# Optimization experiments

Hardware: AMD Instinct MI355X
Metric: run time of the kernel (lower is better)

Reference implementation:

```python
import jax, jax.numpy as jnp
import numpy as np

IN_DIM = 500
BATCH = 131072
NBSECTOR = 11
NBMQ = 10
X_THRESHOLD = 0.001
INF_SCALE = 100.0
ZSTAR = 1000.0
CARD_UPPER = 70.0
CARD_LOWER = 69.0


def setup_inputs() -> dict:
    key = jax.random.key(0)
    ks = jax.random.split(key, 7)
    x = jax.random.uniform(ks[0], (BATCH, IN_DIM), dtype=jnp.float32)
    x_bw = jax.random.uniform(ks[1], (IN_DIM,), dtype=jnp.float32)
    alpha = jax.random.normal(ks[2], (IN_DIM,), dtype=jnp.float32)
    beta = jax.random.normal(ks[3], (IN_DIM,), dtype=jnp.float32)
    # risk matrix: small-magnitude so the quadratic form dQd is in a sane range
    Omega = 0.001 * jax.random.normal(ks[4], (IN_DIM, IN_DIM), dtype=jnp.float32)
    sector_id = jax.random.randint(ks[5], (IN_DIM,), 0, NBSECTOR, dtype=jnp.int32)
    mq_id = jax.random.randint(ks[6], (IN_DIM,), 0, NBMQ, dtype=jnp.int32)
    return {"x": x, "x_bw": x_bw, "alpha": alpha, "beta": beta,
            "Omega": Omega, "sector_id": sector_id, "mq_id": mq_id}


def reference(x, x_bw, alpha, beta, Omega, sector_id, mq_id):
    relu = jax.nn.relu
    d = x - x_bw                      # [B, D]
    abs_d = jnp.abs(d)
    sx = jnp.sum(x, axis=1)           # [B]

    tot = relu(1.0 - sx) + relu(sx - 1.0)
    tot = tot + relu(jnp.sum(abs_d, axis=1) - 0.05)

    # per-group masked sums (replaces the one-hot matvec loops):
    # segment-sum over the feature axis, then |.|, relu, sum over groups.
    sec = jax.ops.segment_sum(d.T, sector_id, num_segments=NBSECTOR).T  # [B, NBSECTOR]
    tot = tot + jnp.sum(relu(jnp.abs(sec) - 0.1), axis=1)
    mqs = jax.ops.segment_sum(d.T, mq_id, num_segments=NBMQ).T          # [B, NBMQ]
    tot = tot + jnp.sum(relu(jnp.abs(mqs) - 0.1), axis=1)

    tot = tot + relu(jnp.abs(d @ beta) - 0.1)

    # eval-mode cardinality constraint (train=False branch): hard count
    nnz = jnp.sum((x > X_THRESHOLD).astype(x.dtype), axis=1)
    tot = tot + relu(nnz - CARD_UPPER) + relu(CARD_LOWER - nnz)

    # NOTE: original sums |d| over the WHOLE batch (scalar), faithfully kept
    l_all = 0.5 * jnp.sum(abs_d)
    tot = tot + relu(0.6 - l_all)

    dQd = jnp.sum((d @ Omega) * d, axis=1)  # quadratic form per row
    tot = tot + relu(dQd - 0.01) + relu(0.0025 - dQd)

    l2 = d @ alpha
    # MONTH == 0 branch of the original
    tot = tot + relu(100.0 * dQd - 100.0 * l2 - ZSTAR)

    fea_probs = relu(1.0 - jnp.tanh(tot / INF_SCALE))
    return fea_probs
```

## Files before the change

### kernel.cpp

```cpp
#include <hip/hip_runtime.h>
#include <hip/hip_bf16.h>

#define D_IN  500
#define BATCH 131072
#define BM    64

typedef unsigned short u16;
typedef unsigned int   u32;
using f32x4  = __attribute__((ext_vector_type(4))) float;
using bf16x8 = __attribute__((ext_vector_type(8))) short;

__device__ __forceinline__ u16 f2bf(float f) {
  u32 b = __builtin_bit_cast(u32, f);
  b += 0x7FFFu + ((b >> 16) & 1u);
  return (u16)(b >> 16);
}
__device__ __forceinline__ float bf2f(u32 hbits) {
  return __builtin_bit_cast(float, hbits << 16);
}

__device__ __forceinline__ float xla_tanh(float z) {
  float xc = fminf(fmaxf(z, -7.90531110764903f), 7.90531110764903f);
  float x2 = xc * xc;
  float p = fmaf(x2, -2.76076847742355e-16f, 2.00018790482477e-13f);
  p = fmaf(x2, p, -8.60467152213735e-11f);
  p = fmaf(x2, p,  5.12229709037114e-08f);
  p = fmaf(x2, p,  1.48572235717979e-05f);
  p = fmaf(x2, p,  6.37261928875436e-04f);
  p = fmaf(x2, p,  4.89352455891786e-03f);
  p = xc * p;
  float q = fmaf(x2, 1.19825839466702e-06f, 1.18534705686654e-04f);
  q = fmaf(x2, q, 2.26843463243900e-03f);
  q = fmaf(x2, q, 4.89352518554385e-03f);
  return (fabsf(z) < 0.0004f) ? z : (p / q);
}

__global__ void disc_prep(const float* __restrict__ Omega,
                          const float* __restrict__ alpha,
                          const float* __restrict__ beta,
                          const float* __restrict__ x_bw,
                          const int* __restrict__ sector_id,
                          const int* __restrict__ mq_id,
                          u16* __restrict__ wsA,
                          float* __restrict__ thr,
                          float* __restrict__ smalls) {
  int idx = blockIdx.x * 256 + threadIdx.x;
  if (idx == 1) smalls[1] = 0.0f;
  if (idx < 512) thr[idx] = (idx < D_IN) ? (0.001f - x_bw[idx]) : 3.0e38f;
  if (blockIdx.x == 0 && threadIdx.x < 64) {
    float s = 0.f;
    for (int c = threadIdx.x; c < D_IN; c += 64) s += x_bw[c];
    #pragma unroll
    for (int m = 1; m < 64; m <<= 1) s += __shfl_xor(s, m, 64);
    if (threadIdx.x == 0) smalls[0] = s;
  }
  if (idx >= 544 * 512) return;
  int blk    = idx >> 9;
  int within = idx & 511;
  int lane   = within >> 3;
  int e      = within & 7;
  int n, j;
  if (blk < 512) {
    int chunk = blk >> 5;
    int nw    = (blk >> 4) & 1;
    int jg    = (blk >> 2) & 3;
    int ks    = blk & 3;
    n = chunk * 32 + nw * 16 + (lane & 15);
    j = jg * 128 + ks * 32 + ((lane >> 4) << 3) + e;
  } else {
    int b4  = blk - 512;
    int sub = b4 >> 2;
    int ks  = b4 & 3;
    int nw = sub >> 2, jg = sub & 3;
    n = 512 + nw * 16 + (lane & 15);
    j = jg * 128 + ks * 32 + ((lane >> 4) << 3) + e;
  }
  float v = 0.0f;
  if (j < D_IN) {
    if (n < D_IN)       v = Omega[j * D_IN + n];
    else if (n < 512)   v = 0.0f;
    else if (n < 523)   v = (sector_id[j] == (n - 512)) ? 1.0f : 0.0f;
    else if (n < 533)   v = (mq_id[j]     == (n - 523)) ? 1.0f : 0.0f;
    else if (n == 533)  v = beta[j];
    else if (n == 534)  v = alpha[j];
    else if (n == 535)  v = 1.0f;
  }
  wsA[idx] = f2bf(v);
}

__global__ __launch_bounds__(512, 2) void disc_main(
    const float* __restrict__ x, const float* __restrict__ x_bw,
    const u16* __restrict__ wsA, const float* __restrict__ thr,
    const float* __restrict__ smalls,
    float* __restrict__ tot_out, float* __restrict__ l_all) {
  __shared__ alignas(16) u16 ldsA[BM * 512];
  __shared__ float s_ext[BM][25];
  __shared__ float s_dqd[BM][8];
  __shared__ float s_sabs[BM];
  __shared__ float s_nnz[BM];

  const int t = threadIdx.x;
  const float* xblk = x + (size_t)blockIdx.x * (BM * D_IN);

  for (int z = t; z < BM * 25; z += 512) ((float*)s_ext)[z] = 0.0f;
  if (t < BM) { s_sabs[t] = 0.0f; s_nnz[t] = 0.0f; }

  for (int z = t; z < BM * 12; z += 512) {
    int r = z / 12, c = 500 + (z - r * 12);
    int byte = ((r << 10) + (c << 1)) ^ ((r & 7) << 4);
    *(u16*)((char*)ldsA + byte) = 0;
  }

  #pragma unroll
  for (int k = 0; k < 16; ++k) {
    int v4 = t + k * 512;
    if (v4 < (BM * D_IN) / 4) {
      int r = (int)(((unsigned)v4 * 33555u) >> 22);
      int c = v4 - r * 125;
      float4 xv = *(const float4*)(xblk + r * D_IN + c * 4);
      float4 bw = *(const float4*)(x_bw + c * 4);
      u32 lo = (u32)f2bf(xv.x - bw.x) | ((u32)f2bf(xv.y - bw.y) << 16);
      u32 hi = (u32)f2bf(xv.z - bw.z) | ((u32)f2bf(xv.w - bw.w) << 16);
      int byte = ((r << 10) + (c << 3)) ^ ((r & 7) << 4);
      *(uint2*)((char*)ldsA + byte) = make_uint2(lo, hi);
    }
  }

  __syncthreads();

  const int l   = t & 63;
  const int w   = t >> 6;
  const int nw  = w >> 2;
  const int jg  = w & 3;
  const int l15 = l & 15;
  const int l4  = l >> 4;
  const f32x4 fzero = {0.f, 0.f, 0.f, 0.f};

  bf16x8 bfs[4][4];
  #pragma unroll
  for (int ks = 0; ks < 4; ++ks) {
    const int kk = jg * 128 + ks * 32 + l4 * 8;
    #pragma unroll
    for (int cf = 0; cf < 4; ++cf) {
      int i = cf * 16 + l15;
      int byte = ((i << 10) + (kk << 1)) ^ ((i & 7) << 4);
      bfs[ks][cf] = *(const bf16x8*)((const char*)ldsA + byte);
    }
  }

  {
    float psab[4] = {0.f, 0.f, 0.f, 0.f};
    float pnnz[4] = {0.f, 0.f, 0.f, 0.f};
    #pragma unroll
    for (int kq = 0; kq < 2; ++kq) {
      const int ks = nw * 2 + kq;
      const int kk = jg * 128 + ks * 32 + l4 * 8;
      float4 th0 = *(const float4*)(thr + kk);
      float4 th1 = *(const float4*)(thr + kk + 4);
      #pragma unroll
      for (int cf = 0; cf < 4; ++cf) {
        bf16x8 bv = bfs[ks][cf];
        #pragma unroll
        for (int e = 0; e < 8; ++e) {
          float dv = bf2f((u32)(u16)bv[e]);
          float th = (e < 4) ? ((const float*)&th0)[e] : ((const float*)&th1)[e - 4];
          psab[cf] += fabsf(dv);
          pnnz[cf] += (dv > th) ? 1.0f : 0.0f;
        }
      }
    }
    #pragma unroll
    for (int cf = 0; cf < 4; ++cf) {
      atomicAdd(&s_sabs[cf * 16 + l15], psab[cf]);
      atomicAdd(&s_nnz[cf * 16 + l15], pnnz[cf]);
    }
  }

  float pdqd[4] = {0.f, 0.f, 0.f, 0.f};
  const u16* wAl = wsA + (l << 3);
  const int fb0 = nw * 16 + jg * 4;

  bf16x8 af[4];
  #pragma unroll
  for (int ks = 0; ks < 4; ++ks)
    af[ks] = *(const bf16x8*)(wAl + ((fb0 + ks) << 9));

  #pragma unroll 1
  for (int chunk = 0; chunk < 16; ++chunk) {
    f32x4 acc[4] = {fzero, fzero, fzero, fzero};
    #pragma unroll
    for (int ks = 0; ks < 4; ++ks)
      #pragma unroll
      for (int cf = 0; cf < 4; ++cf)
        acc[cf] = __builtin_amdgcn_mfma_f32_16x16x32_bf16(af[ks], bfs[ks][cf], acc[cf], 0, 0, 0);
    const int nb = (chunk < 15) ? ((chunk + 1) * 32 + fb0)
                                : (512 + (nw * 4 + jg) * 4);
    #pragma unroll
    for (int ks = 0; ks < 4; ++ks)
      af[ks] = *(const bf16x8*)(wAl + ((nb + ks) << 9));
    const int nbase = chunk * 32 + nw * 16 + l4 * 4;
    #pragma unroll
    for (int cf = 0; cf < 4; ++cf) {
      int i = cf * 16 + l15;
      int byte = ((i << 10) + (nbase << 1)) ^ ((i & 7) << 4);
      uint2 dv = *(const uint2*)((const char*)ldsA + byte);
      pdqd[cf] += acc[cf][0] * bf2f(dv.x & 0xFFFFu)
                + acc[cf][1] * bf2f(dv.x >> 16)
                + acc[cf][2] * bf2f(dv.y & 0xFFFFu)
                + acc[cf][3] * bf2f(dv.y >> 16);
    }
  }

  {
    f32x4 acc4[4];
    #pragma unroll
    for (int cf = 0; cf < 4; ++cf) acc4[cf] = fzero;
    #pragma unroll
    for (int ks = 0; ks < 4; ++ks)
      #pragma unroll
      for (int cf = 0; cf < 4; ++cf)
        acc4[cf] = __builtin_amdgcn_mfma_f32_16x16x32_bf16(af[ks], bfs[ks][cf], acc4[cf], 0, 0, 0);
    #pragma unroll
    for (int cf = 0; cf < 4; ++cf) {
      int i = cf * 16 + l15;
      #pragma unroll
      for (int q = 0; q < 4; ++q) {
        int n = 512 + nw * 16 + l4 * 4 + q;
        if (n < 536) atomicAdd(&s_ext[i][n - 512], acc4[cf][q]);
      }
    }
  }

  #pragma unroll
  for (int cf = 0; cf < 4; ++cf) {
    float v = pdqd[cf];
    v += __shfl_xor(v, 16, 64);
    v += __shfl_xor(v, 32, 64);
    if (l < 16) s_dqd[cf * 16 + l][w] = v;
  }
  __syncthreads();

  if (t < BM) {
    float dqd = 0.f;
    #pragma unroll
    for (int ww = 0; ww < 8; ++ww) dqd += s_dqd[t][ww];
    float tex = 0.f;
    #pragma unroll
    for (int c = 0; c < 22; ++c)
      tex += fmaxf(fabsf(s_ext[t][c]) - 0.1f, 0.f);
    float l2 = s_ext[t][22];
    float sx = s_ext[t][23] + smalls[0];
    float sabs = s_sabs[t], nnz = s_nnz[t];
    float tot = tex
      + fmaxf(1.f - sx, 0.f) + fmaxf(sx - 1.f, 0.f)
      + fmaxf(sabs - 0.05f, 0.f)
      + fmaxf(nnz - 70.f, 0.f) + fmaxf(69.f - nnz, 0.f)
      + fmaxf(dqd - 0.01f, 0.f) + fmaxf(0.0025f - dqd, 0.f)
      + fmaxf(100.f * dqd - 100.f * l2 - 1000.f, 0.f);
    tot_out[(size_t)blockIdx.x * BM + t] = tot;
    float bs = sabs;
    #pragma unroll
    for (int m = 1; m < 64; m <<= 1) bs += __shfl_xor(bs, m, 64);
    if (t == 0) atomicAdd(l_all, bs);
  }
}

__global__ void disc_final(const float* __restrict__ tot_in,
                           const float* __restrict__ l_all,
                           float* __restrict__ out) {
  int i = blockIdx.x * 256 + threadIdx.x;
  if (i >= BATCH) return;
  float lterm = fmaxf(0.6f - 0.5f * (*l_all), 0.0f);
  float z = (tot_in[i] + lterm) * 0.01f;
  out[i] = fmaxf(1.0f - xla_tanh(z), 0.0f);
}

extern "C" void kernel_launch(void* const* d_in, const int* in_sizes, int n_in,
                              void* d_out, int out_size, void* d_ws, size_t ws_size,
                              hipStream_t stream) {
  const float* x     = (const float*)d_in[0];
  const float* x_bw  = (const float*)d_in[1];
  const float* alpha = (const float*)d_in[2];
  const float* beta  = (const float*)d_in[3];
  const float* Omega = (const float*)d_in[4];
  const int* sector_id = (const int*)d_in[5];
  const int* mq_id     = (const int*)d_in[6];
  float* out = (float*)d_out;

  char* ws = (char*)d_ws;
  u16*   wsA    = (u16*)ws;
  float* thr    = (float*)(ws + 544 * 1024);
  float* smalls = (float*)(ws + 544 * 1024 + 2048);
  float* tot    = (float*)(ws + 544 * 1024 + 4096);

  disc_prep<<<1088, 256, 0, stream>>>(Omega, alpha, beta, x_bw, sector_id, mq_id,
                                      wsA, thr, smalls);
  disc_main<<<BATCH / BM, 512, 0, stream>>>(x, x_bw, wsA, thr, smalls,
                                            tot, smalls + 1);
  disc_final<<<BATCH / 256, 256, 0, stream>>>(tot, smalls + 1, out);
}
```

Baseline: 567.2 us.

## Double-buffer weight fragments, raise occupancy, and use nontemporal x loads

Raises the launch-bounds minimum from 2 to 4 blocks per CU, so the compiler must cap registers for more resident waves. It loads x with nontemporal hints and issues the first weight-fragment loads before the barrier. The MFMA loop now double-buffers the A fragments (afA/afB) across two chunks per iteration, so global loads for the next chunk overlap compute on the current one. The stats loop is split by wave group with scalar threshold loads. The 64KB LDS tile per block likely limits residency whatever the launch bound says, and the tighter register cap with extra fragment buffers risks spills.

```diff
diff --git a/kernel.cpp b/kernel.cpp
--- a/kernel.cpp
+++ b/kernel.cpp
@@ -88,7 +88,7 @@
   wsA[idx] = f2bf(v);
 }
 
-__global__ __launch_bounds__(512, 2) void disc_main(
+__global__ __launch_bounds__(512, 4) void disc_main(
     const float* __restrict__ x, const float* __restrict__ x_bw,
     const u16* __restrict__ wsA, const float* __restrict__ thr,
     const float* __restrict__ smalls,
@@ -117,16 +117,14 @@
     if (v4 < (BM * D_IN) / 4) {
       int r = (int)(((unsigned)v4 * 33555u) >> 22);
       int c = v4 - r * 125;
-      float4 xv = *(const float4*)(xblk + r * D_IN + c * 4);
-      float4 bw = *(const float4*)(x_bw + c * 4);
-      u32 lo = (u32)f2bf(xv.x - bw.x) | ((u32)f2bf(xv.y - bw.y) << 16);
-      u32 hi = (u32)f2bf(xv.z - bw.z) | ((u32)f2bf(xv.w - bw.w) << 16);
+      f32x4 xv = __builtin_nontemporal_load((const f32x4*)(xblk + r * D_IN + c * 4));
+      f32x4 bw = *(const f32x4*)(x_bw + c * 4);
+      u32 lo = (u32)f2bf(xv[0] - bw[0]) | ((u32)f2bf(xv[1] - bw[1]) << 16);
+      u32 hi = (u32)f2bf(xv[2] - bw[2]) | ((u32)f2bf(xv[3] - bw[3]) << 16);
       int byte = ((r << 10) + (c << 3)) ^ ((r & 7) << 4);
       *(uint2*)((char*)ldsA + byte) = make_uint2(lo, hi);
     }
   }
-
-  __syncthreads();
 
   const int l   = t & 63;
   const int w   = t >> 6;
@@ -135,6 +133,15 @@
   const int l15 = l & 15;
   const int l4  = l >> 4;
   const f32x4 fzero = {0.f, 0.f, 0.f, 0.f};
+  const u16* wAl = wsA + (l << 3);
+  const int fb0 = nw * 16 + jg * 4;
+
+  bf16x8 afA[4], afB[4];
+  #pragma unroll
+  for (int ks = 0; ks < 4; ++ks)
+    afA[ks] = *(const bf16x8*)(wAl + ((fb0 + ks) << 9));
+
+  __syncthreads();
 
   bf16x8 bfs[4][4];
   #pragma unroll
@@ -151,24 +158,26 @@
   {
     float psab[4] = {0.f, 0.f, 0.f, 0.f};
     float pnnz[4] = {0.f, 0.f, 0.f, 0.f};
-    #pragma unroll
-    for (int kq = 0; kq < 2; ++kq) {
-      const int ks = nw * 2 + kq;
-      const int kk = jg * 128 + ks * 32 + l4 * 8;
-      float4 th0 = *(const float4*)(thr + kk);
-      float4 th1 = *(const float4*)(thr + kk + 4);
-      #pragma unroll
-      for (int cf = 0; cf < 4; ++cf) {
-        bf16x8 bv = bfs[ks][cf];
-        #pragma unroll
-        for (int e = 0; e < 8; ++e) {
-          float dv = bf2f((u32)(u16)bv[e]);
-          float th = (e < 4) ? ((const float*)&th0)[e] : ((const float*)&th1)[e - 4];
-          psab[cf] += fabsf(dv);
-          pnnz[cf] += (dv > th) ? 1.0f : 0.0f;
-        }
-      }
-    }
+#define STATS_KS(KS)                                                        \
+    {                                                                       \
+      const int kk = jg * 128 + (KS) * 32 + l4 * 8;                         \
+      float th[8];                                                          \
+      _Pragma("unroll")                                                     \
+      for (int e = 0; e < 8; ++e) th[e] = thr[kk + e];                      \
+      _Pragma("unroll")                                                     \
+      for (int cf = 0; cf < 4; ++cf) {                                      \
+        bf16x8 bv = bfs[KS][cf];                                            \
+        _Pragma("unroll")                                                   \
+        for (int e = 0; e < 8; ++e) {                                       \
+          float dv = bf2f((u32)(u16)bv[e]);                                 \
+          psab[cf] += fabsf(dv);                                            \
+          pnnz[cf] += (dv > th[e]) ? 1.0f : 0.0f;                           \
+        }                                                                   \
+      }                                                                     \
+    }
+    if (nw == 0) { STATS_KS(0) STATS_KS(1) }
+    else         { STATS_KS(2) STATS_KS(3) }
+#undef STATS_KS
     #pragma unroll
     for (int cf = 0; cf < 4; ++cf) {
       atomicAdd(&s_sabs[cf * 16 + l15], psab[cf]);
@@ -177,49 +186,55 @@
   }
 
   float pdqd[4] = {0.f, 0.f, 0.f, 0.f};
-  const u16* wAl = wsA + (l << 3);
-  const int fb0 = nw * 16 + jg * 4;
-
-  bf16x8 af[4];
-  #pragma unroll
-  for (int ks = 0; ks < 4; ++ks)
-    af[ks] = *(const bf16x8*)(wAl + ((fb0 + ks) << 9));
+
+#define MFMA_CHUNK(AF, ACC)                                                 \
+    _Pragma("unroll")                                                       \
+    for (int ks = 0; ks < 4; ++ks)                                          \
+      _Pragma("unroll")                                                     \
+      for (int cf = 0; cf < 4; ++cf)                                        \
+        ACC[cf] = __builtin_amdgcn_mfma_f32_16x16x32_bf16(AF[ks], bfs[ks][cf], ACC[cf], 0, 0, 0);
+
+#define EPILOGUE(CHUNK, ACC)                                                \
+    {                                                                       \
+      const int nbase = (CHUNK) * 32 + nw * 16 + l4 * 4;                    \
+      _Pragma("unroll")                                                     \
+      for (int cf = 0; cf < 4; ++cf) {                                      \
+        int i = cf * 16 + l15;                                              \
+        int byte = ((i << 10) + (nbase << 1)) ^ ((i & 7) << 4);             \
+        uint2 dv = *(const uint2*)((const char*)ldsA + byte);               \
+        pdqd[cf] += ACC[cf][0] * bf2f(dv.x & 0xFFFFu)                       \
+                  + ACC[cf][1] * bf2f(dv.x >> 16)                           \
+                  + ACC[cf][2] * bf2f(dv.y & 0xFFFFu)                       \
+                  + ACC[cf][3] * bf2f(dv.y >> 16);                          \
+      }                                                                     \
+    }
 
   #pragma unroll 1
-  for (int chunk = 0; chunk < 16; ++chunk) {
-    f32x4 acc[4] = {fzero, fzero, fzero, fzero};
-    #pragma unroll
-    for (int ks = 0; ks < 4; ++ks)
+  for (int c2 = 0; c2 < 8; ++c2) {
+    {
+      const int nb = (2 * c2 + 1) * 32 + fb0;
       #pragma unroll
-      for (int cf = 0; cf < 4; ++cf)
-        acc[cf] = __builtin_amdgcn_mfma_f32_16x16x32_bf16(af[ks], bfs[ks][cf], acc[cf], 0, 0, 0);
-    const int nb = (chunk < 15) ? ((chunk + 1) * 32 + fb0)
-                                : (512 + (nw * 4 + jg) * 4);
-    #pragma unroll
-    for (int ks = 0; ks < 4; ++ks)
-      af[ks] = *(const bf16x8*)(wAl + ((nb + ks) << 9));
-    const int nbase = chunk * 32 + nw * 16 + l4 * 4;
-    #pragma unroll
-    for (int cf = 0; cf < 4; ++cf) {
-      int i = cf * 16 + l15;
-      int byte = ((i << 10) + (nbase << 1)) ^ ((i & 7) << 4);
-      uint2 dv = *(const uint2*)((const char*)ldsA + byte);
-      pdqd[cf] += acc[cf][0] * bf2f(dv.x & 0xFFFFu)
-                + acc[cf][1] * bf2f(dv.x >> 16)
-                + acc[cf][2] * bf2f(dv.y & 0xFFFFu)
-                + acc[cf][3] * bf2f(dv.y >> 16);
+      for (int ks = 0; ks < 4; ++ks)
+        afB[ks] = *(const bf16x8*)(wAl + ((nb + ks) << 9));
+      f32x4 acc[4] = {fzero, fzero, fzero, fzero};
+      MFMA_CHUNK(afA, acc)
+      EPILOGUE(2 * c2, acc)
+    }
+    {
+      const int nb = (c2 < 7) ? ((2 * c2 + 2) * 32 + fb0)
+                              : (512 + (nw * 4 + jg) * 4);
+      #pragma unroll
+      for (int ks = 0; ks < 4; ++ks)
+        afA[ks] = *(const bf16x8*)(wAl + ((nb + ks) << 9));
+      f32x4 acc[4] = {fzero, fzero, fzero, fzero};
+      MFMA_CHUNK(afB, acc)
+      EPILOGUE(2 * c2 + 1, acc)
     }
   }
 
   {
-    f32x4 acc4[4];
-    #pragma unroll
-    for (int cf = 0; cf < 4; ++cf) acc4[cf] = fzero;
-    #pragma unroll
-    for (int ks = 0; ks < 4; ++ks)
-      #pragma unroll
-      for (int cf = 0; cf < 4; ++cf)
-        acc4[cf] = __builtin_amdgcn_mfma_f32_16x16x32_bf16(af[ks], bfs[ks][cf], acc4[cf], 0, 0, 0);
+    f32x4 acc4[4] = {fzero, fzero, fzero, fzero};
+    MFMA_CHUNK(afA, acc4)
     #pragma unroll
     for (int cf = 0; cf < 4; ++cf) {
       int i = cf * 16 + l15;
@@ -230,6 +245,8 @@
       }
     }
   }
+#undef MFMA_CHUNK
+#undef EPILOGUE
 
   #pragma unroll
   for (int cf = 0; cf < 4; ++cf) {
```

Result: slower. 586.6 us (+3.4%).
